# Kernel tuning notes

Measured on AMD Instinct MI355X. Metric: run time of the kernel, lower is better.

## Reference

```python
import jax, jax.numpy as jnp
import numpy as np

B_SZ = 16
L = 256
D_MODEL = 256
D_STATE = 16
D_CONV = 4
EXPAND = 2
D_INNER = EXPAND * D_MODEL  # 512
DT_RANK = (D_MODEL + 15) // 16  # 16
TARGET_LEN = 16


def setup_inputs() -> dict:
    key = jax.random.key(0)
    ks = jax.random.split(key, 10)
    s = 0.02
    x = jax.random.normal(ks[0], (B_SZ, D_MODEL, L), dtype=jnp.float32)
    W_in = jax.random.normal(ks[1], (2 * D_INNER, D_MODEL), dtype=jnp.float32) * s
    conv_w = jax.random.normal(ks[2], (D_INNER, D_CONV), dtype=jnp.float32) * s
    conv_b = jax.random.normal(ks[3], (D_INNER,), dtype=jnp.float32) * s
    W_x = jax.random.normal(ks[4], (DT_RANK + 2 * D_STATE, D_INNER), dtype=jnp.float32) * s
    W_dt = jax.random.normal(ks[5], (D_INNER, DT_RANK), dtype=jnp.float32) * s
    b_dt = jax.random.normal(ks[6], (D_INNER,), dtype=jnp.float32) * s
    # canonical Mamba A init: A_log = log(1..d_state) per channel
    A_log = jnp.log(jnp.tile(jnp.arange(1, D_STATE + 1, dtype=jnp.float32), (D_INNER, 1)))
    Dp = jnp.ones((D_INNER,), dtype=jnp.float32)
    W_out = jax.random.normal(ks[7], (D_MODEL, D_INNER), dtype=jnp.float32) * s
    return {"x": x, "W_in": W_in, "conv_w": conv_w, "conv_b": conv_b,
            "W_x": W_x, "W_dt": W_dt, "b_dt": b_dt, "A_log": A_log,
            "Dp": Dp, "W_out": W_out}


def _selective_scan(u, delta, A, Bm, Cm, Dp):
    # u, delta: [B,L,d_in]; Bm, Cm: [B,L,N]; A: [d_in,N]; Dp: [d_in]
    dA = jnp.exp(delta[..., None] * A)                                  # [B,L,d_in,N]
    dBu = delta[..., None] * Bm[:, :, None, :] * u[..., None]           # [B,L,d_in,N]

    def step(h, t):
        dA_t, dBu_t, C_t = t                                            # [B,d_in,N],[B,d_in,N],[B,N]
        h = dA_t * h + dBu_t
        y = jnp.einsum('bdn,bn->bd', h, C_t)
        return h, y

    h0 = jnp.zeros((u.shape[0], u.shape[2], A.shape[1]), u.dtype)
    _, ys = jax.lax.scan(step, h0,
                         (dA.transpose(1, 0, 2, 3), dBu.transpose(1, 0, 2, 3),
                          Cm.transpose(1, 0, 2)))
    return ys.transpose(1, 0, 2) + u * Dp                               # [B,L,d_in]


def _mamba(xt, W_in, conv_w, conv_b, W_x, W_dt, b_dt, A_log, Dp, W_out):
    # xt: [B,L,D_MODEL]
    xz = xt @ W_in.T                                                    # [B,L,2*d_in]
    xi, z = jnp.split(xz, 2, axis=-1)
    # causal depthwise conv1d over L
    xc = xi.transpose(0, 2, 1)                                          # [B,d_in,L]
    xc = jax.lax.conv_general_dilated(
        xc, conv_w[:, None, :], (1,), [(D_CONV - 1, 0)],
        dimension_numbers=('NCH', 'OIH', 'NCH'), feature_group_count=D_INNER)
    xi = jax.nn.silu((xc + conv_b[None, :, None]).transpose(0, 2, 1))   # [B,L,d_in]
    x_dbl = xi @ W_x.T                                                  # [B,L,dt_rank+2N]
    dt, Bm, Cm = jnp.split(x_dbl, [DT_RANK, DT_RANK + D_STATE], axis=-1)
    delta = jax.nn.softplus(dt @ W_dt.T + b_dt)                         # [B,L,d_in]
    A = -jnp.exp(A_log)                                                 # [d_in,N]
    y = _selective_scan(xi, delta, A, Bm, Cm, Dp)
    y = y * jax.nn.silu(z)
    return y @ W_out.T                                                  # [B,L,D_MODEL]


def reference(x, W_in, conv_w, conv_b, W_x, W_dt, b_dt, A_log, Dp, W_out):
    inp = x.transpose(0, 2, 1)                                          # [B,L,D]
    outs = []
    for _ in range(TARGET_LEN):
        o = _mamba(inp, W_in, conv_w, conv_b, W_x, W_dt, b_dt, A_log, Dp, W_out)[:, -1:, :]
        outs.append(o)
        inp = jnp.concatenate([inp[:, 1:, :], o], axis=1)
    return jnp.concatenate(outs, axis=1).transpose(0, 2, 1)             # [B,D,target_len]
```

## Files before the change

kernel.cpp:

```cpp
#include <hip/hip_runtime.h>
#include <cmath>

#define DEV __device__ __forceinline__

constexpr int B_SZ = 16;
constexpr int LSEQ = 256;
constexpr int DM   = 256;
constexpr int DI   = 512;
constexpr int TLEN = 16;

DEV float silu_f(float x)     { return x / (1.f + __expf(-x)); }
DEV float softplus_f(float x) { return log1pf(__expf(x)); }

__global__ __launch_bounds__(256) void k_prefill_a(const float* __restrict__ x,
                                                   const float* __restrict__ W_in,
                                                   const float* __restrict__ W_out,
                                                   float* __restrict__ WcT,
                                                   float* __restrict__ xi_pre) {
    __shared__ float smem[2][32][68];
    const int tid = threadIdx.x;
    const int ty = tid >> 4, tx = tid & 15;
    float acc[4][4] = {};
    if (blockIdx.x < 128) {
        const int j0 = (int)(blockIdx.x & 15) * 64;
        const int d0 = (int)(blockIdx.x >> 4) * 64;
        float (*As)[68] = smem[0];
        float (*Bs)[68] = smem[1];
        for (int kc = 0; kc < DM; kc += 32) {
            for (int it = 0; it < 8; ++it) {
                int idx = it * 256 + tid;
                int jj = idx >> 5, kk = idx & 31;
                As[kk][jj] = W_in[(size_t)(j0 + jj) * DM + kc + kk];
            }
            for (int it = 0; it < 8; ++it) {
                int idx = it * 256 + tid;
                int kk = idx >> 6, dd = idx & 63;
                Bs[kk][dd] = W_out[(size_t)(kc + kk) * DI + d0 + dd];
            }
            __syncthreads();
            for (int kk = 0; kk < 32; ++kk) {
                float4 a4 = *(const float4*)&As[kk][ty * 4];
                float4 b4 = *(const float4*)&Bs[kk][tx * 4];
                float av[4] = {a4.x, a4.y, a4.z, a4.w};
                float bv[4] = {b4.x, b4.y, b4.z, b4.w};
                for (int i = 0; i < 4; ++i)
                    for (int j = 0; j < 4; ++j) acc[i][j] = fmaf(av[i], bv[j], acc[i][j]);
            }
            __syncthreads();
        }
        float (*Cs)[65] = (float(*)[65])&smem[0][0][0];
        for (int i = 0; i < 4; ++i)
            for (int j = 0; j < 4; ++j)
                Cs[ty * 4 + i][tx * 4 + j] = acc[i][j];
        __syncthreads();
        const int dr = tid >> 2, jq = tid & 3;
        for (int ii = 0; ii < 4; ++ii) {
            int jl = jq * 16 + ii * 4;
            int jg = j0 + jl;
            int newc;
            if (jg < DI) newc = (jg >> 5) * 64 + (jg & 31);
            else { int jz = jg - DI; newc = (jz >> 5) * 64 + 32 + (jz & 31); }
            float4 v = make_float4(Cs[jl][dr], Cs[jl + 1][dr], Cs[jl + 2][dr], Cs[jl + 3][dr]);
            *(float4*)&WcT[(size_t)(d0 + dr) * 1024 + newc] = v;
        }
    } else {
        const int bid2 = (int)blockIdx.x - 128;
        const int bx = bid2 & 7, by = bid2 >> 3;
        const int row0 = by * 64;
        const int b = row0 >> 8, l0 = row0 & 255;
        const int j0 = bx * 64;
        float (*As)[68] = smem[0];
        float (*Ws)[68] = smem[1];
        const float* xb = x + (size_t)b * DM * LSEQ;
        for (int kc = 0; kc < DM; kc += 32) {
            for (int it = 0; it < 8; ++it) {
                int idx = it * 256 + tid;
                int kk = idx >> 6, li = idx & 63;
                As[kk][li] = xb[(kc + kk) * LSEQ + l0 + li];
            }
            for (int it = 0; it < 8; ++it) {
                int idx = it * 256 + tid;
                int jj = idx >> 5, kk = idx & 31;
                Ws[kk][jj] = W_in[(size_t)(j0 + jj) * DM + kc + kk];
            }
            __syncthreads();
            for (int kk = 0; kk < 32; ++kk) {
                float4 a4 = *(const float4*)&As[kk][ty * 4];
                float4 w4 = *(const float4*)&Ws[kk][tx * 4];
                float av[4] = {a4.x, a4.y, a4.z, a4.w};
                float wv[4] = {w4.x, w4.y, w4.z, w4.w};
                for (int i = 0; i < 4; ++i)
                    for (int j = 0; j < 4; ++j) acc[i][j] = fmaf(av[i], wv[j], acc[i][j]);
            }
            __syncthreads();
        }
        for (int i = 0; i < 4; ++i) {
            float4 v = make_float4(acc[i][0], acc[i][1], acc[i][2], acc[i][3]);
            *(float4*)&xi_pre[(size_t)(row0 + ty * 4 + i) * DI + j0 + tx * 4] = v;
        }
    }
}

__global__ __launch_bounds__(512) void k_prefill_b(const float* __restrict__ xi_pre,
                                                   const float* __restrict__ conv_w,
                                                   const float* __restrict__ conv_b,
                                                   const float* __restrict__ W_x,
                                                   const float* __restrict__ W_dt,
                                                   const float* __restrict__ b_dt,
                                                   const float* __restrict__ A_log,
                                                   float* __restrict__ Qb,
                                                   float* __restrict__ Sb,
                                                   float* __restrict__ dtBC255) {
    __shared__ float As[32][516];
    __shared__ float Ws[48][129];
    __shared__ float dt_s[32][49];
    const int blk = blockIdx.x;
    const int b = blk >> 3, c = blk & 7;
    const int d = threadIdx.x;
    const int l0 = c * 32;
    {
        const float c0 = conv_w[d * 4 + 0], c1 = conv_w[d * 4 + 1];
        const float c2 = conv_w[d * 4 + 2], c3 = conv_w[d * 4 + 3];
        const float cbv = conv_b[d];
        float p0, p1, p2;
        int l;
        l = l0 - 3; p0 = (l >= 0) ? xi_pre[(size_t)(b * 256 + l) * DI + d] : 0.f;
        l = l0 - 2; p1 = (l >= 0) ? xi_pre[(size_t)(b * 256 + l) * DI + d] : 0.f;
        l = l0 - 1; p2 = (l >= 0) ? xi_pre[(size_t)(b * 256 + l) * DI + d] : 0.f;
        for (int ll = 0; ll < 32; ++ll) {
            float v = xi_pre[(size_t)(b * 256 + l0 + ll) * DI + d];
            As[ll][d] = silu_f(cbv + c0 * p0 + c1 * p1 + c2 * p2 + c3 * v);
            p0 = p1; p1 = p2; p2 = v;
        }
    }
    __syncthreads();
    {
        const int lr = d >> 4, rg = d & 15;
        float acc[3] = {};
        for (int kc = 0; kc < 4; ++kc) {
            for (int it = 0; it < 12; ++it) {
                int idx = it * 512 + d;
                int rr = idx >> 7, k = idx & 127;
                Ws[rr][k] = W_x[(size_t)rr * DI + kc * 128 + k];
            }
            __syncthreads();
            for (int k = 0; k < 128; ++k) {
                float a = As[lr][kc * 128 + k];
                acc[0] = fmaf(a, Ws[rg * 3 + 0][k], acc[0]);
                acc[1] = fmaf(a, Ws[rg * 3 + 1][k], acc[1]);
                acc[2] = fmaf(a, Ws[rg * 3 + 2][k], acc[2]);
            }
            __syncthreads();
        }
        dt_s[lr][rg * 3 + 0] = acc[0];
        dt_s[lr][rg * 3 + 1] = acc[1];
        dt_s[lr][rg * 3 + 2] = acc[2];
    }
    __syncthreads();
    {
        float Ar[16], Wd[16];
        for (int n = 0; n < 16; ++n) Ar[n] = -__expf(A_log[d * 16 + n]);
        for (int r = 0; r < 16; ++r) Wd[r] = W_dt[d * 16 + r];
        const float bd = b_dt[d];
        float q[16] = {};
        float Ssum = 0.f;
        for (int l = 0; l < 32; ++l) {
            float s = bd;
            for (int r = 0; r < 16; ++r) s = fmaf(dt_s[l][r], Wd[r], s);
            const float del = softplus_f(s);
            const float u = As[l][d];
            const float du = del * u;
            Ssum += del;
            for (int n = 0; n < 16; ++n) {
                float dA = __expf(del * Ar[n]);
                q[n] = fmaf(dA, q[n], du * dt_s[l][16 + n]);
            }
        }
        float* qo = Qb + ((size_t)blk * DI + d) * 16;
        for (int n = 0; n < 16; ++n) qo[n] = q[n];
        Sb[blk * DI + d] = Ssum;
    }
    if (c == 7 && d < 48) dtBC255[b * 48 + d] = dt_s[31][d];
}

__global__ __launch_bounds__(512) void k_prefill_c(const float* __restrict__ x,
                                                   const float* __restrict__ W_in,
                                                   const float* __restrict__ Qb,
                                                   const float* __restrict__ Sb,
                                                   const float* __restrict__ dtBC255,
                                                   const float* __restrict__ xi_pre,
                                                   const float* __restrict__ conv_w,
                                                   const float* __restrict__ conv_b,
                                                   const float* __restrict__ A_log,
                                                   const float* __restrict__ Dp,
                                                   float* __restrict__ h_state,
                                                   float* __restrict__ gbuf) {
    __shared__ __align__(16) float xcol[256];
    const int b = blockIdx.x;
    const int d = threadIdx.x;
    if (d < 256) xcol[d] = x[(size_t)b * DM * LSEQ + d * LSEQ + 255];
    __syncthreads();
    float z = 0.f;
    {
        const float4* wr = (const float4*)&W_in[(size_t)(DI + d) * DM];
        const float4* xc4 = (const float4*)xcol;
        for (int k = 0; k < 64; ++k) {
            float4 w = wr[k], xx = xc4[k];
            z += w.x * xx.x + w.y * xx.y + w.z * xx.z + w.w * xx.w;
        }
    }
    float Ar[16];
    for (int n = 0; n < 16; ++n) Ar[n] = -__expf(A_log[d * 16 + n]);
    float h[16] = {};
    for (int c = 0; c < 8; ++c) {
        const int blk = b * 8 + c;
        const float S = Sb[blk * DI + d];
        const float* qv = Qb + ((size_t)blk * DI + d) * 16;
        for (int n = 0; n < 16; ++n) {
            float P = __expf(S * Ar[n]);
            h[n] = fmaf(P, h[n], qv[n]);
        }
    }
    float y = 0.f;
    for (int n = 0; n < 16; ++n) y = fmaf(h[n], dtBC255[b * 48 + 32 + n], y);
    float u;
    {
        float s = conv_b[d];
        for (int k = 0; k < 4; ++k)
            s = fmaf(conv_w[d * 4 + k], xi_pre[(size_t)(b * 256 + 252 + k) * DI + d], s);
        u = silu_f(s);
    }
    y = fmaf(u, Dp[d], y);
    gbuf[b * DI + d] = y * silu_f(z);
    float* ho = h_state + ((size_t)(b * DI + d)) * 16;
    for (int n = 0; n < 16; ++n) ho[n] = h[n];
}

__global__ __launch_bounds__(512, 2) void k_gen(
    const float* __restrict__ WcT, const float* __restrict__ W_out,
    const float* __restrict__ W_x, const float* __restrict__ W_dt,
    const float* __restrict__ conv_w, const float* __restrict__ conv_b,
    const float* __restrict__ b_dt, const float* __restrict__ A_log,
    const float* __restrict__ Dp, const float* __restrict__ xi_pre,
    const float* __restrict__ h_state, const float* __restrict__ gbuf0,
    float* __restrict__ xbuf, unsigned* __restrict__ flags,
    float* __restrict__ out) {
    const int bid = blockIdx.x;
    const int b = bid & 15;
    const int p = bid >> 4;
    const int tid = threadIdx.x;

    __shared__ float wx_s[48][517];
    __shared__ float gs_s[512];
    __shared__ float xin_s[512];
    __shared__ float zs_s[512];
    __shared__ float red8[8][65];
    __shared__ float dtbc_s[48];
    __shared__ float hist[3][32];

    const int r = tid & 63, w = tid >> 6;
    float wc[64];
    {
        const float* src = WcT + (size_t)(w * 64) * 1024 + p * 64 + r;
        #pragma unroll
        for (int kk = 0; kk < 64; ++kk) wc[kk] = src[(size_t)kk * 1024];
    }
    #pragma unroll
    for (int kk = 0; kk < 64; ++kk) asm volatile("" : "+v"(wc[kk]));

    for (int it = 0; it < 48; ++it) {
        int flat = it * 512 + tid;
        wx_s[flat >> 9][flat & 511] = W_x[flat];
    }
    const int orow = p * 16 + (tid >> 5), osub = tid & 31;
    float wout[16];
    #pragma unroll
    for (int j = 0; j < 16; ++j) wout[j] = W_out[(size_t)orow * DI + osub + 32 * j];
    #pragma unroll
    for (int j = 0; j < 16; ++j) asm volatile("" : "+v"(wout[j]));

    float wdt[16], Ar[16], h[16];
    {
        const float4* wp = (const float4*)&W_dt[tid * 16];
        const float4* ap = (const float4*)&A_log[tid * 16];
        const float4* hp = (const float4*)&h_state[((size_t)(b * DI + tid)) * 16];
        #pragma unroll
        for (int i = 0; i < 4; ++i) {
            float4 wv = wp[i], av = ap[i], hv = hp[i];
            wdt[4*i+0]=wv.x; wdt[4*i+1]=wv.y; wdt[4*i+2]=wv.z; wdt[4*i+3]=wv.w;
            Ar[4*i+0]=-__expf(av.x); Ar[4*i+1]=-__expf(av.y);
            Ar[4*i+2]=-__expf(av.z); Ar[4*i+3]=-__expf(av.w);
            h[4*i+0]=hv.x; h[4*i+1]=hv.y; h[4*i+2]=hv.z; h[4*i+3]=hv.w;
        }
    }
    #pragma unroll
    for (int i = 0; i < 16; ++i) asm volatile("" : "+v"(wdt[i]));
    const float bd = b_dt[tid];
    const float Dpv = Dp[tid];
    float cw0 = 0, cw1 = 0, cw2 = 0, cw3 = 0, cb = 0;
    if (tid < 32) {
        const int d = p * 32 + tid;
        cw0 = conv_w[d * 4 + 0]; cw1 = conv_w[d * 4 + 1];
        cw2 = conv_w[d * 4 + 2]; cw3 = conv_w[d * 4 + 3];
        cb  = conv_b[d];
        for (int k = 0; k < 3; ++k)
            hist[k][tid] = xi_pre[(size_t)(b * 256 + 253 + k) * DI + d];
    }
    gs_s[tid] = gbuf0[b * DI + tid];
    __syncthreads();

    for (int t = 0; t < TLEN; ++t) {
        if (t < TLEN - 1) {
            {
                const float4* g4 = (const float4*)&gs_s[w * 64];
                float s = 0.f;
                #pragma unroll
                for (int kk = 0; kk < 16; ++kk) {
                    float4 g = g4[kk];
                    s = fmaf(wc[4*kk+0], g.x, s);
                    s = fmaf(wc[4*kk+1], g.y, s);
                    s = fmaf(wc[4*kk+2], g.z, s);
                    s = fmaf(wc[4*kk+3], g.w, s);
                }
                red8[w][r] = s;
            }
            __syncthreads();
            if (tid < 64) {
                float v = 0.f;
                #pragma unroll
                for (int ss = 0; ss < 8; ++ss) v += red8[ss][tid];
                float outv;
                if (tid < 32) {
                    float xc = cb;
                    xc = fmaf(cw0, hist[t % 3][tid], xc);
                    xc = fmaf(cw1, hist[(t + 1) % 3][tid], xc);
                    xc = fmaf(cw2, hist[(t + 2) % 3][tid], xc);
                    xc = fmaf(cw3, v, xc);
                    hist[t % 3][tid] = v;
                    outv = silu_f(xc);
                } else {
                    outv = v;
                }
                __hip_atomic_store(&xbuf[((size_t)((b * 16 + p) * 2 + (t & 1))) * 64 + tid],
                                   outv, __ATOMIC_RELAXED, __HIP_MEMORY_SCOPE_AGENT);
            }
            __syncthreads();
            if (tid == 0)
                __hip_atomic_store(&flags[b * 16 + p], (unsigned)(t + 1),
                                   __ATOMIC_RELEASE, __HIP_MEMORY_SCOPE_AGENT);
        }
        {
            float s = 0.f;
            #pragma unroll
            for (int j = 0; j < 16; ++j) s = fmaf(wout[j], gs_s[osub + 32 * j], s);
            s += __shfl_down(s, 16); s += __shfl_down(s, 8);
            s += __shfl_down(s, 4);  s += __shfl_down(s, 2); s += __shfl_down(s, 1);
            if (osub == 0) out[(size_t)(b * 256 + orow) * TLEN + t] = s;
        }
        if (t == TLEN - 1) return;

        if (tid < 16) {
            while (__hip_atomic_load(&flags[b * 16 + tid],
                                     __ATOMIC_ACQUIRE, __HIP_MEMORY_SCOPE_AGENT)
                   < (unsigned)(t + 1))
                __builtin_amdgcn_s_sleep(1);
        }
        __syncthreads();
        #pragma unroll
        for (int i = 0; i < 2; ++i) {
            int idx = i * 512 + tid;
            int q = idx >> 6, pos = idx & 63;
            float v = __hip_atomic_load(
                xbuf + ((size_t)((b * 16 + q) * 2 + (t & 1))) * 64 + pos,
                __ATOMIC_RELAXED, __HIP_MEMORY_SCOPE_AGENT);
            if (pos < 32) xin_s[q * 32 + pos] = v;
            else          zs_s[q * 32 + pos - 32] = v;
        }
        __syncthreads();
        {
            const int rr = tid & 63, ks = tid >> 6;
            float s = 0.f;
            if (rr < 48) {
                const float* wr = &wx_s[rr][ks * 64];
                const float* xv = &xin_s[ks * 64];
                #pragma unroll
                for (int k = 0; k < 64; ++k) s = fmaf(wr[k], xv[k], s);
            }
            red8[ks][rr] = s;
        }
        __syncthreads();
        if (tid < 48) {
            float s = 0.f;
            #pragma unroll
            for (int ss = 0; ss < 8; ++ss) s += red8[ss][tid];
            dtbc_s[tid] = s;
        }
        __syncthreads();
        {
            float dt_l = bd;
            #pragma unroll
            for (int rr = 0; rr < 16; ++rr) dt_l = fmaf(dtbc_s[rr], wdt[rr], dt_l);
            const float del = softplus_f(dt_l);
            const float u = xin_s[tid];
            const float du = del * u;
            float y = 0.f;
            #pragma unroll
            for (int n = 0; n < 16; ++n) {
                float dA = __expf(del * Ar[n]);
                h[n] = fmaf(dA, h[n], du * dtbc_s[16 + n]);
                y = fmaf(h[n], dtbc_s[32 + n], y);
            }
            y = fmaf(u, Dpv, y);
            gs_s[tid] = y * silu_f(zs_s[tid]);
        }
        __syncthreads();
    }
}

extern "C" void kernel_launch(void* const* d_in, const int* in_sizes, int n_in,
                              void* d_out, int out_size, void* d_ws, size_t ws_size,
                              hipStream_t stream) {
    const float* x      = (const float*)d_in[0];
    const float* W_in   = (const float*)d_in[1];
    const float* conv_w = (const float*)d_in[2];
    const float* conv_b = (const float*)d_in[3];
    const float* W_x    = (const float*)d_in[4];
    const float* W_dt   = (const float*)d_in[5];
    const float* b_dt   = (const float*)d_in[6];
    const float* A_log  = (const float*)d_in[7];
    const float* Dp     = (const float*)d_in[8];
    const float* W_out  = (const float*)d_in[9];
    float* out = (float*)d_out;

    float* base = (float*)d_ws;
    size_t off = 0;
    auto alloc = [&](size_t n) { float* pp = base + off; off += (n + 15) & ~(size_t)15; return pp; };
    unsigned* flags = (unsigned*)alloc(256);
    float* xbuf     = alloc((size_t)16 * 16 * 2 * 64);
    float* gbuf     = alloc(16 * 512);
    float* h_state  = alloc((size_t)16 * 512 * 16);
    float* dtBC255  = alloc(16 * 48);
    float* Sb       = alloc((size_t)128 * 512);
    float* Qb       = alloc((size_t)128 * 512 * 16);
    float* xi_pre   = alloc((size_t)4096 * 512);
    float* WcT      = alloc((size_t)512 * 1024);

    hipMemsetAsync(flags, 0, 256 * sizeof(unsigned), stream);
    hipLaunchKernelGGL(k_prefill_a, dim3(640), dim3(256), 0, stream,
                       x, W_in, W_out, WcT, xi_pre);
    hipLaunchKernelGGL(k_prefill_b, dim3(128), dim3(512), 0, stream,
                       xi_pre, conv_w, conv_b, W_x, W_dt, b_dt, A_log, Qb, Sb, dtBC255);
    hipLaunchKernelGGL(k_prefill_c, dim3(16), dim3(512), 0, stream,
                       x, W_in, Qb, Sb, dtBC255, xi_pre, conv_w, conv_b, A_log, Dp,
                       h_state, gbuf);
    hipLaunchKernelGGL(k_gen, dim3(256), dim3(512), 0, stream,
                       WcT, W_out, W_x, W_dt, conv_w, conv_b, b_dt, A_log, Dp,
                       xi_pre, h_state, gbuf, xbuf, flags, out);
}
```

Baseline: 339.7 us.

## Distribute W_x projection across producer blocks and exchange partial dt/B/C sums

```diff
diff --git a/kernel.cpp b/kernel.cpp
--- a/kernel.cpp
+++ b/kernel.cpp
@@ -250,35 +250,39 @@
     const int p = bid >> 4;
     const int tid = threadIdx.x;
 
-    __shared__ float wx_s[48][517];
-    __shared__ float gs_s[512];
+    __shared__ float wxp[48][37];
+    __shared__ float wout_s[16][516];
+    __shared__ __align__(16) float gs_s[512];
     __shared__ float xin_s[512];
     __shared__ float zs_s[512];
-    __shared__ float red8[8][65];
-    __shared__ float dtbc_s[48];
+    __shared__ float red8[8][68];
+    __shared__ float dpart[16][52];
+    __shared__ __align__(16) float dtbc_s[48];
+    __shared__ float post_s[112];
     __shared__ float hist[3][32];
 
-    const int r = tid & 63, w = tid >> 6;
-    float wc[64];
-    {
-        const float* src = WcT + (size_t)(w * 64) * 1024 + p * 64 + r;
-        #pragma unroll
-        for (int kk = 0; kk < 64; ++kk) wc[kk] = src[(size_t)kk * 1024];
-    }
-    #pragma unroll
-    for (int kk = 0; kk < 64; ++kk) asm volatile("" : "+v"(wc[kk]));
-
-    for (int it = 0; it < 48; ++it) {
+    for (int it = 0; it < 3; ++it) {
         int flat = it * 512 + tid;
-        wx_s[flat >> 9][flat & 511] = W_x[flat];
-    }
-    const int orow = p * 16 + (tid >> 5), osub = tid & 31;
-    float wout[16];
-    #pragma unroll
-    for (int j = 0; j < 16; ++j) wout[j] = W_out[(size_t)orow * DI + osub + 32 * j];
-    #pragma unroll
-    for (int j = 0; j < 16; ++j) asm volatile("" : "+v"(wout[j]));
-
+        int rr = flat >> 5, cc = flat & 31;
+        wxp[rr][cc] = W_x[(size_t)rr * DI + p * 32 + cc];
+    }
+    for (int it = 0; it < 16; ++it) {
+        int flat = it * 512 + tid;
+        int row = flat >> 9, col = flat & 511;
+        wout_s[row][col] = W_out[(size_t)(p * 16 + row) * DI + col];
+    }
+    const float bd = b_dt[tid];
+    const float Dpv = Dp[tid];
+    float cw0 = 0, cw1 = 0, cw2 = 0, cw3 = 0, cb = 0;
+    if (tid < 32) {
+        const int d = p * 32 + tid;
+        cw0 = conv_w[d * 4 + 0]; cw1 = conv_w[d * 4 + 1];
+        cw2 = conv_w[d * 4 + 2]; cw3 = conv_w[d * 4 + 3];
+        cb  = conv_b[d];
+        for (int k = 0; k < 3; ++k)
+            hist[k][tid] = xi_pre[(size_t)(b * 256 + 253 + k) * DI + d];
+    }
+    gs_s[tid] = gbuf0[b * DI + tid];
     float wdt[16], Ar[16], h[16];
     {
         const float4* wp = (const float4*)&W_dt[tid * 16];
@@ -295,18 +299,20 @@
     }
     #pragma unroll
     for (int i = 0; i < 16; ++i) asm volatile("" : "+v"(wdt[i]));
-    const float bd = b_dt[tid];
-    const float Dpv = Dp[tid];
-    float cw0 = 0, cw1 = 0, cw2 = 0, cw3 = 0, cb = 0;
-    if (tid < 32) {
-        const int d = p * 32 + tid;
-        cw0 = conv_w[d * 4 + 0]; cw1 = conv_w[d * 4 + 1];
-        cw2 = conv_w[d * 4 + 2]; cw3 = conv_w[d * 4 + 3];
-        cb  = conv_b[d];
-        for (int k = 0; k < 3; ++k)
-            hist[k][tid] = xi_pre[(size_t)(b * 256 + 253 + k) * DI + d];
-    }
-    gs_s[tid] = gbuf0[b * DI + tid];
+
+    __builtin_amdgcn_sched_barrier(0);
+    const int r = tid & 63, w = tid >> 6;
+    float wc[64];
+    {
+        const float* src = WcT + (size_t)(w * 64) * 1024 + p * 64 + r;
+        #pragma unroll
+        for (int kk = 0; kk < 64; ++kk) wc[kk] = src[(size_t)kk * 1024];
+    }
+    #pragma unroll
+    for (int kk = 0; kk < 64; ++kk) asm volatile("" : "+v"(wc[kk]));
+    __builtin_amdgcn_sched_barrier(0);
+
+    const int orow_l = tid >> 5, osub = tid & 31;
     __syncthreads();
 
     for (int t = 0; t < TLEN; ++t) {
@@ -329,7 +335,6 @@
                 float v = 0.f;
                 #pragma unroll
                 for (int ss = 0; ss < 8; ++ss) v += red8[ss][tid];
-                float outv;
                 if (tid < 32) {
                     float xc = cb;
                     xc = fmaf(cw0, hist[t % 3][tid], xc);
@@ -337,12 +342,24 @@
                     xc = fmaf(cw2, hist[(t + 2) % 3][tid], xc);
                     xc = fmaf(cw3, v, xc);
                     hist[t % 3][tid] = v;
-                    outv = silu_f(xc);
+                    post_s[tid] = silu_f(xc);
                 } else {
-                    outv = v;
+                    post_s[tid] = v;
                 }
-                __hip_atomic_store(&xbuf[((size_t)((b * 16 + p) * 2 + (t & 1))) * 64 + tid],
-                                   outv, __ATOMIC_RELAXED, __HIP_MEMORY_SCOPE_AGENT);
+            }
+            __syncthreads();
+            if (tid < 384) {
+                const int rr = tid >> 3, q = tid & 7;
+                const float* wr = &wxp[rr][q * 4];
+                const float* xv = &post_s[q * 4];
+                float s = wr[0]*xv[0] + wr[1]*xv[1] + wr[2]*xv[2] + wr[3]*xv[3];
+                s += __shfl_down(s, 4); s += __shfl_down(s, 2); s += __shfl_down(s, 1);
+                if (q == 0) post_s[64 + rr] = s;
+            }
+            __syncthreads();
+            if (tid < 112) {
+                __hip_atomic_store(&xbuf[((size_t)((b * 16 + p) * 2 + (t & 1))) * 128 + tid],
+                                   post_s[tid], __ATOMIC_RELAXED, __HIP_MEMORY_SCOPE_AGENT);
             }
             __syncthreads();
             if (tid == 0)
@@ -352,63 +369,71 @@
         {
             float s = 0.f;
             #pragma unroll
-            for (int j = 0; j < 16; ++j) s = fmaf(wout[j], gs_s[osub + 32 * j], s);
+            for (int j = 0; j < 16; ++j)
+                s = fmaf(wout_s[orow_l][osub + 32 * j], gs_s[osub + 32 * j], s);
             s += __shfl_down(s, 16); s += __shfl_down(s, 8);
             s += __shfl_down(s, 4);  s += __shfl_down(s, 2); s += __shfl_down(s, 1);
-            if (osub == 0) out[(size_t)(b * 256 + orow) * TLEN + t] = s;
+            if (osub == 0) out[(size_t)(b * 256 + p * 16 + orow_l) * TLEN + t] = s;
         }
         if (t == TLEN - 1) return;
 
         if (tid < 16) {
             while (__hip_atomic_load(&flags[b * 16 + tid],
-                                     __ATOMIC_ACQUIRE, __HIP_MEMORY_SCOPE_AGENT)
+                                     __ATOMIC_RELAXED, __HIP_MEMORY_SCOPE_AGENT)
                    < (unsigned)(t + 1))
                 __builtin_amdgcn_s_sleep(1);
         }
         __syncthreads();
+        __builtin_amdgcn_fence(__ATOMIC_ACQUIRE, "agent");
         #pragma unroll
-        for (int i = 0; i < 2; ++i) {
+        for (int i = 0; i < 4; ++i) {
             int idx = i * 512 + tid;
-            int q = idx >> 6, pos = idx & 63;
-            float v = __hip_atomic_load(
-                xbuf + ((size_t)((b * 16 + q) * 2 + (t & 1))) * 64 + pos,
-                __ATOMIC_RELAXED, __HIP_MEMORY_SCOPE_AGENT);
-            if (pos < 32) xin_s[q * 32 + pos] = v;
-            else          zs_s[q * 32 + pos - 32] = v;
-        }
-        __syncthreads();
-        {
-            const int rr = tid & 63, ks = tid >> 6;
-            float s = 0.f;
-            if (rr < 48) {
-                const float* wr = &wx_s[rr][ks * 64];
-                const float* xv = &xin_s[ks * 64];
-                #pragma unroll
-                for (int k = 0; k < 64; ++k) s = fmaf(wr[k], xv[k], s);
-            }
-            red8[ks][rr] = s;
+            int q = idx >> 7, pos = idx & 127;
+            if (pos < 112) {
+                float v = __hip_atomic_load(
+                    xbuf + ((size_t)((b * 16 + q) * 2 + (t & 1))) * 128 + pos,
+                    __ATOMIC_RELAXED, __HIP_MEMORY_SCOPE_AGENT);
+                if (pos < 32)      xin_s[q * 32 + pos] = v;
+                else if (pos < 64) zs_s[q * 32 + pos - 32] = v;
+                else               dpart[q][pos - 64] = v;
+            }
         }
         __syncthreads();
         if (tid < 48) {
             float s = 0.f;
             #pragma unroll
-            for (int ss = 0; ss < 8; ++ss) s += red8[ss][tid];
+            for (int q = 0; q < 16; ++q) s += dpart[q][tid];
             dtbc_s[tid] = s;
         }
         __syncthreads();
         {
+            const float4* dt4 = (const float4*)dtbc_s;
             float dt_l = bd;
             #pragma unroll
-            for (int rr = 0; rr < 16; ++rr) dt_l = fmaf(dtbc_s[rr], wdt[rr], dt_l);
+            for (int i = 0; i < 4; ++i) {
+                float4 dv = dt4[i];
+                dt_l = fmaf(dv.x, wdt[4*i+0], dt_l);
+                dt_l = fmaf(dv.y, wdt[4*i+1], dt_l);
+                dt_l = fmaf(dv.z, wdt[4*i+2], dt_l);
+                dt_l = fmaf(dv.w, wdt[4*i+3], dt_l);
+            }
             const float del = softplus_f(dt_l);
             const float u = xin_s[tid];
             const float du = del * u;
             float y = 0.f;
             #pragma unroll
-            for (int n = 0; n < 16; ++n) {
-                float dA = __expf(del * Ar[n]);
-                h[n] = fmaf(dA, h[n], du * dtbc_s[16 + n]);
-                y = fmaf(h[n], dtbc_s[32 + n], y);
+            for (int nq = 0; nq < 4; ++nq) {
+                float4 Bv = dt4[4 + nq];
+                float4 Cv = dt4[8 + nq];
+                float bb[4] = {Bv.x, Bv.y, Bv.z, Bv.w};
+                float cc[4] = {Cv.x, Cv.y, Cv.z, Cv.w};
+                #pragma unroll
+                for (int j = 0; j < 4; ++j) {
+                    const int n = nq * 4 + j;
+                    float dA = __expf(del * Ar[n]);
+                    h[n] = fmaf(dA, h[n], du * bb[j]);
+                    y = fmaf(h[n], cc[j], y);
+                }
             }
             y = fmaf(u, Dpv, y);
             gs_s[tid] = y * silu_f(zs_s[tid]);
@@ -436,7 +461,7 @@
     size_t off = 0;
     auto alloc = [&](size_t n) { float* pp = base + off; off += (n + 15) & ~(size_t)15; return pp; };
     unsigned* flags = (unsigned*)alloc(256);
-    float* xbuf     = alloc((size_t)16 * 16 * 2 * 64);
+    float* xbuf     = alloc((size_t)16 * 16 * 2 * 128);
     float* gbuf     = alloc(16 * 512);
     float* h_state  = alloc((size_t)16 * 512 * 16);
     float* dtBC255  = alloc(16 * 48);
```

Result: slower. 522.1 us (+53.7%).
